# Optimization experiments

Measured on AMD Instinct MI355X. Metric: run time of the kernel, lower is better.

## Reference

```python
import jax, jax.numpy as jnp
import numpy as np

N_NODES = 20000
N_EDGES = 100000
IN = 512
HID = 512
OUT = 512
EF = 128
NH = 16
HEAD = OUT // NH


def _ln(x):
    mu = jnp.mean(x, axis=-1, keepdims=True)
    var = jnp.var(x, axis=-1, keepdims=True)
    return (x - mu) / jnp.sqrt(var + 1e-5)


def _mlp(x, W1, b1, g, be, W2, b2):
    hdn = x @ W1 + b1
    hdn = _ln(hdn) * g + be
    hdn = jax.nn.relu(hdn)
    return hdn @ W2 + b2


def setup_inputs() -> dict:
    key = jax.random.key(0)
    ks = jax.random.split(key, 16)

    def w(k, i, o):
        return jax.random.normal(k, (i, o), jnp.float32) / np.float32(np.sqrt(i))

    inp = {
        'h': jax.random.normal(ks[0], (N_NODES, IN), jnp.float32),
        'edge_feat': jax.random.normal(ks[1], (N_EDGES, EF), jnp.float32),
        'edge_index': jax.random.randint(ks[2], (2, N_EDGES), 0, N_NODES, jnp.int32),
    }
    # hk / hv MLPs: kv_input_dim = IN + EF
    inp['hk_W1'] = w(ks[3], IN + EF, HID); inp['hk_b1'] = jnp.zeros((HID,), jnp.float32)
    inp['hk_g'] = jnp.ones((HID,), jnp.float32); inp['hk_be'] = jnp.zeros((HID,), jnp.float32)
    inp['hk_W2'] = w(ks[4], HID, OUT); inp['hk_b2'] = jnp.zeros((OUT,), jnp.float32)
    inp['hv_W1'] = w(ks[5], IN + EF, HID); inp['hv_b1'] = jnp.zeros((HID,), jnp.float32)
    inp['hv_g'] = jnp.ones((HID,), jnp.float32); inp['hv_be'] = jnp.zeros((HID,), jnp.float32)
    inp['hv_W2'] = w(ks[6], HID, OUT); inp['hv_b2'] = jnp.zeros((OUT,), jnp.float32)
    # hq MLP: input_dim -> output_dim
    inp['hq_W1'] = w(ks[7], IN, HID); inp['hq_b1'] = jnp.zeros((HID,), jnp.float32)
    inp['hq_g'] = jnp.ones((HID,), jnp.float32); inp['hq_be'] = jnp.zeros((HID,), jnp.float32)
    inp['hq_W2'] = w(ks[8], HID, OUT); inp['hq_b2'] = jnp.zeros((OUT,), jnp.float32)
    # node_output MLP: 2*hidden -> hidden
    inp['no_W1'] = w(ks[9], 2 * HID, HID); inp['no_b1'] = jnp.zeros((HID,), jnp.float32)
    inp['no_g'] = jnp.ones((HID,), jnp.float32); inp['no_be'] = jnp.zeros((HID,), jnp.float32)
    inp['no_W2'] = w(ks[10], HID, HID); inp['no_b2'] = jnp.zeros((HID,), jnp.float32)
    return inp


def reference(h, edge_feat, edge_index,
              hk_W1, hk_b1, hk_g, hk_be, hk_W2, hk_b2,
              hv_W1, hv_b1, hv_g, hv_be, hv_W2, hv_b2,
              hq_W1, hq_b1, hq_g, hq_be, hq_W2, hq_b2,
              no_W1, no_b1, no_g, no_be, no_W2, no_b2):
    N = h.shape[0]
    src, dst = edge_index[0], edge_index[1]
    # edge gather + per-edge K/V MLPs
    kv_in = jnp.concatenate([h[src], edge_feat], axis=-1)          # [E, IN+EF]
    k = _mlp(kv_in, hk_W1, hk_b1, hk_g, hk_be, hk_W2, hk_b2).reshape(-1, NH, HEAD)
    v = _mlp(kv_in, hv_W1, hv_b1, hv_g, hv_be, hv_W2, hv_b2).reshape(-1, NH, HEAD)
    q = _mlp(h, hq_W1, hq_b1, hq_g, hq_be, hq_W2, hq_b2).reshape(-1, NH, HEAD)
    # scatter softmax over incoming edges of each dst node
    logits = jnp.sum(q[dst] * k, axis=-1) / np.float32(np.sqrt(HEAD))  # [E, NH]
    mx = jax.ops.segment_max(logits, dst, num_segments=N)              # [N, NH]
    ex = jnp.exp(logits - mx[dst])
    den = jax.ops.segment_sum(ex, dst, num_segments=N)                 # [N, NH]
    alpha = ex / den[dst]                                              # [E, NH]
    # scatter-sum aggregate
    m = alpha[..., None] * v                                           # [E, NH, HEAD]
    out = jax.ops.segment_sum(m, dst, num_segments=N).reshape(N, OUT)
    out = _mlp(jnp.concatenate([out, h], axis=-1), no_W1, no_b1, no_g, no_be, no_W2, no_b2)
    return out + h
```

## Files before the change

kernel.cpp:

```cpp
#include <hip/hip_runtime.h>

#define NN 20000
#define NE 100000

typedef unsigned short u16;
typedef __bf16 bf16x8 __attribute__((ext_vector_type(8)));
typedef float f32x4 __attribute__((ext_vector_type(4)));
typedef short short8 __attribute__((ext_vector_type(8)));
typedef u16 u16x4 __attribute__((ext_vector_type(4)));

__device__ __forceinline__ float bf2f(u16 u) {
    union { unsigned int i; float f; } x; x.i = ((unsigned int)u) << 16; return x.f;
}
__device__ __forceinline__ u16 f2bf(float f) {
    union { float f; unsigned int i; } x; x.f = f;
    unsigned int r = x.i + 0x7FFFu + ((x.i >> 16) & 1u);
    return (u16)(r >> 16);
}

__device__ __forceinline__ void gl_lds16(const void* g, void* l) {
    __builtin_amdgcn_global_load_lds(
        (__attribute__((address_space(1))) const void*)g,
        (__attribute__((address_space(3))) void*)l, 16, 0, 0);
}

__global__ void cvt_k(const float* __restrict__ in, u16* __restrict__ out, long n) {
    long i = ((long)blockIdx.x * 256 + threadIdx.x) * 4;
    if (i < n) {
        f32x4 v = *(const f32x4*)(in + i);
        u16x4 o;
        #pragma unroll
        for (int j = 0; j < 4; j++) o[j] = f2bf(v[j]);
        *(u16x4*)(out + i) = o;
    }
}

__global__ __launch_bounds__(256)
void ttr_k(const float* __restrict__ W, u16* __restrict__ WT, int Kr) {
    __shared__ float tile[32][33];
    int k0 = blockIdx.x * 32, n0 = blockIdx.y * 32;
    int tx = threadIdx.x & 31, ty = threadIdx.x >> 5;
    #pragma unroll
    for (int i = 0; i < 4; i++)
        tile[ty + 8 * i][tx] = W[(size_t)(k0 + ty + 8 * i) * 512 + n0 + tx];
    __syncthreads();
    #pragma unroll
    for (int i = 0; i < 4; i++)
        WT[(size_t)(n0 + ty + 8 * i) * Kr + k0 + tx] = f2bf(tile[tx][ty + 8 * i]);
}

template<int AK, bool BIAS, bool DEVM, bool OUTF, bool LOGIT>
__global__ __launch_bounds__(256, 2)
void gemm_k(const u16* __restrict__ A, const u16* __restrict__ A2,
            const int* __restrict__ eids, const int* __restrict__ Be, int ci, int cap,
            const u16* __restrict__ WT, const float* __restrict__ bias,
            void* __restrict__ Cv,
            const u16* __restrict__ qbv, const int* __restrict__ dstv, float* __restrict__ lgv,
            int Mh, int K, int Ast, int Cst)
{
    __shared__ u16 smem[128 * 128];
    u16* sA = smem;
    u16* sB = smem + 128 * 64;
    int M = Mh, b0 = 0;
    if constexpr (DEVM) {
        b0 = Be[ci];
        M = min(Be[ci + 1] - b0, cap);
    }
    const int m0 = blockIdx.y * 128;
    if (m0 >= M) return;
    const int t = threadIdx.x;
    const int n0 = blockIdx.x * 128;
    const int lane = t & 63;
    const int w = t >> 6;
    const int lrow = lane >> 3;
    const int swz = ((lane & 7) ^ lrow) * 8;
    const int ldst = w * 512 + lane * 8;

    size_t abase[4];
    #pragma unroll
    for (int p = 0; p < 4; p++) {
        int row = min(m0 + p * 32 + w * 8 + lrow, M - 1);
        if constexpr (AK == 2) abase[p] = (size_t)row * 512;
        else                   abase[p] = (size_t)row * Ast;
    }
    const int wm = w >> 1, wn = w & 1;
    const int lm = lane & 15, lk = lane >> 4;
    const int swzr = lm & 7;

    f32x4 acc[4][4] = {};

    for (int k0 = 0; k0 < K; k0 += 64) {
        #pragma unroll
        for (int p = 0; p < 4; p++) {
            const u16* g;
            if constexpr (AK == 2) {
                g = (k0 < 512) ? (A + abase[p] + k0 + swz) : (A2 + abase[p] + (k0 - 512) + swz);
            } else {
                g = A + abase[p] + k0 + swz;
            }
            gl_lds16(g, sA + p * 2048 + ldst);
        }
        #pragma unroll
        for (int p = 0; p < 4; p++)
            gl_lds16(WT + (size_t)(n0 + p * 32 + w * 8 + lrow) * K + k0 + swz, sB + p * 2048 + ldst);
        __syncthreads();

        bf16x8 av[2][4], bv[2][4];
        #pragma unroll
        for (int hf = 0; hf < 2; hf++) {
            #pragma unroll
            for (int mi = 0; mi < 4; mi++)
                av[hf][mi] = *(const bf16x8*)(sA + (wm * 64 + mi * 16 + lm) * 64 + (((hf * 4 + lk) ^ swzr) * 8));
            #pragma unroll
            for (int ni = 0; ni < 4; ni++)
                bv[hf][ni] = *(const bf16x8*)(sB + (wn * 64 + ni * 16 + lm) * 64 + (((hf * 4 + lk) ^ swzr) * 8));
        }
        #pragma unroll
        for (int hf = 0; hf < 2; hf++)
            #pragma unroll
            for (int mi = 0; mi < 4; mi++)
                #pragma unroll
                for (int ni = 0; ni < 4; ni++)
                    acc[mi][ni] = __builtin_amdgcn_mfma_f32_16x16x32_bf16(av[hf][mi], bv[hf][ni], acc[mi][ni], 0, 0, 0);
        __syncthreads();
    }

    float bvv[4];
    #pragma unroll
    for (int ni = 0; ni < 4; ni++) bvv[ni] = BIAS ? bias[n0 + wn * 64 + ni * 16 + lm] : 0.f;

    if constexpr (LOGIT) {
        const int qrow = t >> 4;
        const int qc = t & 15;
        #pragma unroll
        for (int p = 0; p < 8; p++) {
            int row = p * 16 + qrow;
            int grow = min(m0 + row, M - 1);
            int e = eids[b0 + grow];
            const u16* g = qbv + (size_t)dstv[e] * 512 + n0 + ((qc ^ (row & 7)) << 3);
            gl_lds16(g, smem + p * 2048 + t * 8);
        }
        __syncthreads();
        #pragma unroll
        for (int mi = 0; mi < 4; mi++) {
            #pragma unroll
            for (int r = 0; r < 4; r++) {
                int rloc = wm * 64 + mi * 16 + lk * 4 + r;
                float h0 = 0.f, h1 = 0.f;
                #pragma unroll
                for (int ni = 0; ni < 4; ni++) {
                    int cloc = wn * 64 + ni * 16 + lm;
                    int addr = rloc * 128 + ((((cloc >> 3) ^ (rloc & 7)) << 3) | (cloc & 7));
                    float qv = bf2f(smem[addr]);
                    float pr = (acc[mi][ni][r] + bvv[ni]) * qv;
                    if (ni < 2) h0 += pr; else h1 += pr;
                }
                #pragma unroll
                for (int o = 1; o < 16; o <<= 1) { h0 += __shfl_xor(h0, o); h1 += __shfl_xor(h1, o); }
                int grow = m0 + rloc;
                if (lm == 0 && grow < M) {
                    int hbase = (n0 >> 5) + wn * 2;
                    lgv[(size_t)(b0 + grow) * 16 + hbase]     = h0 * 0.17677669529663687f;
                    lgv[(size_t)(b0 + grow) * 16 + hbase + 1] = h1 * 0.17677669529663687f;
                }
            }
        }
        return;
    }

    #pragma unroll
    for (int mi = 0; mi < 4; mi++) {
        int rbase = m0 + wm * 64 + mi * 16 + lk * 4;
        #pragma unroll
        for (int ni = 0; ni < 4; ni++) {
            int n = n0 + wn * 64 + ni * 16 + lm;
            #pragma unroll
            for (int r = 0; r < 4; r++) {
                int row = rbase + r;
                if (row < M) {
                    float cv = acc[mi][ni][r] + bvv[ni];
                    if constexpr (OUTF) ((float*)Cv)[(size_t)row * Cst + n] = cv;
                    else                ((u16*)Cv)[(size_t)row * Cst + n] = f2bf(cv);
                }
            }
        }
    }
}

template<int AK, bool BIAS, bool RES, bool OUTF, bool RESB>
__global__ __launch_bounds__(256, 3)
void gemmS_k(const u16* __restrict__ A, const u16* __restrict__ A2,
             const u16* __restrict__ WT, const float* __restrict__ bias,
             const float* __restrict__ resid, void* __restrict__ Cv,
             int M, int K, int Ast, int Cst)
{
    __shared__ u16 sA[64 * 64];
    __shared__ u16 sB[128 * 64];
    const int m0 = blockIdx.y * 64;
    if (m0 >= M) return;
    const int t = threadIdx.x;
    const int n0 = blockIdx.x * 128;
    const int lane = t & 63;
    const int w = t >> 6;
    const int lrow = lane >> 3;
    const int swz = ((lane & 7) ^ lrow) * 8;
    const int ldst = w * 512 + lane * 8;

    size_t abase[2];
    #pragma unroll
    for (int p = 0; p < 2; p++) {
        int row = min(m0 + p * 32 + w * 8 + lrow, M - 1);
        if constexpr (AK == 2) abase[p] = (size_t)row * 512;
        else                   abase[p] = (size_t)row * Ast;
    }
    const int wm = w >> 1, wn = w & 1;
    const int lm = lane & 15, lk = lane >> 4;
    const int swzr = lm & 7;

    f32x4 acc[2][4] = {};

    for (int k0 = 0; k0 < K; k0 += 64) {
        #pragma unroll
        for (int p = 0; p < 2; p++) {
            const u16* g;
            if constexpr (AK == 2) {
                g = (k0 < 512) ? (A + abase[p] + k0 + swz) : (A2 + abase[p] + (k0 - 512) + swz);
            } else {
                g = A + abase[p] + k0 + swz;
            }
            gl_lds16(g, sA + p * 2048 + ldst);
        }
        #pragma unroll
        for (int p = 0; p < 4; p++)
            gl_lds16(WT + (size_t)(n0 + p * 32 + w * 8 + lrow) * K + k0 + swz, sB + p * 2048 + ldst);
        __syncthreads();

        bf16x8 av[2][2], bv[2][4];
        #pragma unroll
        for (int hf = 0; hf < 2; hf++) {
            #pragma unroll
            for (int mi = 0; mi < 2; mi++)
                av[hf][mi] = *(const bf16x8*)(sA + (wm * 32 + mi * 16 + lm) * 64 + (((hf * 4 + lk) ^ swzr) * 8));
            #pragma unroll
            for (int ni = 0; ni < 4; ni++)
                bv[hf][ni] = *(const bf16x8*)(sB + (wn * 64 + ni * 16 + lm) * 64 + (((hf * 4 + lk) ^ swzr) * 8));
        }
        #pragma unroll
        for (int hf = 0; hf < 2; hf++)
            #pragma unroll
            for (int mi = 0; mi < 2; mi++)
                #pragma unroll
                for (int ni = 0; ni < 4; ni++)
                    acc[mi][ni] = __builtin_amdgcn_mfma_f32_16x16x32_bf16(av[hf][mi], bv[hf][ni], acc[mi][ni], 0, 0, 0);
        __syncthreads();
    }

    float bvv[4];
    #pragma unroll
    for (int ni = 0; ni < 4; ni++) bvv[ni] = BIAS ? bias[n0 + wn * 64 + ni * 16 + lm] : 0.f;
    #pragma unroll
    for (int mi = 0; mi < 2; mi++) {
        int rbase = m0 + wm * 32 + mi * 16 + lk * 4;
        #pragma unroll
        for (int ni = 0; ni < 4; ni++) {
            int n = n0 + wn * 64 + ni * 16 + lm;
            #pragma unroll
            for (int r = 0; r < 4; r++) {
                int row = rbase + r;
                if (row < M) {
                    float cv = acc[mi][ni][r] + bvv[ni];
                    if constexpr (RES) {
                        if constexpr (RESB) cv += bf2f(((const u16*)resid)[(size_t)row * 512 + n]);
                        else                cv += resid[(size_t)row * 512 + n];
                    }
                    if constexpr (OUTF) ((float*)Cv)[(size_t)row * Cst + n] = cv;
                    else                ((u16*)Cv)[(size_t)row * Cst + n] = f2bf(cv);
                }
            }
        }
    }
}

__global__ __launch_bounds__(256, 2)
void g1ln_k(const u16* __restrict__ efb, const u16* __restrict__ WTe,
            const u16* __restrict__ NPp, const int* __restrict__ eids, const int* __restrict__ srcv,
            const int* __restrict__ Be, int ci, int cap,
            const float* __restrict__ b1, const float* __restrict__ g, const float* __restrict__ be,
            u16* __restrict__ outb)
{
    __shared__ u16 lds[4096 + 16384];
    u16* sA = lds;
    u16* sB = lds + 4096;
    float* sC = (float*)(lds + 4096);
    int b0 = Be[ci];
    int M = min(Be[ci + 1] - b0, cap);
    const int m0 = blockIdx.x * 32;
    if (m0 >= M) return;
    const int t = threadIdx.x;
    const int lane = t & 63;
    const int w = t >> 6;
    const int lm = lane & 15, lk = lane >> 4;

    #pragma unroll
    for (int p = 0; p < 2; p++) {
        int slot = p * 256 + t;
        int row = slot >> 4, gph = slot & 15;
        int gsrc = (gph & 8) | ((gph & 7) ^ (row & 7));
        int eid = eids[b0 + min(m0 + row, M - 1)];
        gl_lds16(efb + (size_t)eid * 128 + gsrc * 8, sA + slot * 8);
    }

    f32x4 acc[2][8] = {};
    for (int ks = 0; ks < 4; ks++) {
        #pragma unroll
        for (int p = 0; p < 8; p++) {
            int slot = p * 256 + t;
            int n = slot >> 2, cph = slot & 3;
            int csrc = cph ^ (n & 3);
            gl_lds16(WTe + (size_t)n * 128 + ks * 32 + csrc * 8, sB + slot * 8);
        }
        __syncthreads();
        bf16x8 av[2], bv[8];
        #pragma unroll
        for (int mi = 0; mi < 2; mi++) {
            int row = mi * 16 + lm;
            int gl = ks * 4 + lk;
            int gph = (gl & 8) | ((gl & 7) ^ (row & 7));
            av[mi] = *(const bf16x8*)(sA + row * 128 + gph * 8);
        }
        #pragma unroll
        for (int ni = 0; ni < 8; ni++) {
            int n = w * 128 + ni * 16 + lm;
            int cph = lk ^ (n & 3);
            bv[ni] = *(const bf16x8*)(sB + n * 32 + cph * 8);
        }
        #pragma unroll
        for (int mi = 0; mi < 2; mi++)
            #pragma unroll
            for (int ni = 0; ni < 8; ni++)
                acc[mi][ni] = __builtin_amdgcn_mfma_f32_16x16x32_bf16(av[mi], bv[ni], acc[mi][ni], 0, 0, 0);
        __syncthreads();
    }

    for (int half = 0; half < 2; half++) {
        #pragma unroll
        for (int ni = 0; ni < 8; ni++) {
            int col = w * 128 + ni * 16 + lm;
            int c4 = col >> 2;
            #pragma unroll
            for (int r = 0; r < 4; r++) {
                int row_l = lk * 4 + r;
                int ph4 = (c4 & ~7) | ((c4 & 7) ^ (row_l & 7));
                sC[row_l * 512 + ph4 * 4 + (col & 3)] = acc[half][ni][r];
            }
        }
        __syncthreads();
        #pragma unroll
        for (int i = 0; i < 4; i++) {
            int row_l = w * 4 + i;
            int row_g = m0 + half * 16 + row_l;
            if (row_g < M) {
                int g0 = lane * 2, g1 = g0 + 1;
                int p0 = (g0 & ~7) | ((g0 & 7) ^ (row_l & 7));
                int p1 = (g1 & ~7) | ((g1 & 7) ^ (row_l & 7));
                f32x4 ca = *(const f32x4*)(sC + row_l * 512 + p0 * 4);
                f32x4 cb = *(const f32x4*)(sC + row_l * 512 + p1 * 4);
                int eid = eids[b0 + row_g];
                const u16* gp = NPp + (size_t)srcv[eid] * 1536 + lane * 8;
                short8 gv = *(const short8*)gp;
                float x[8]; float s = 0.f, s2 = 0.f;
                #pragma unroll
                for (int j = 0; j < 4; j++) x[j] = ca[j] + bf2f((u16)gv[j]) + b1[lane * 8 + j];
                #pragma unroll
                for (int j = 4; j < 8; j++) x[j] = cb[j - 4] + bf2f((u16)gv[j]) + b1[lane * 8 + j];
                #pragma unroll
                for (int j = 0; j < 8; j++) { s += x[j]; s2 += x[j] * x[j]; }
                #pragma unroll
                for (int o = 32; o > 0; o >>= 1) { s += __shfl_xor(s, o); s2 += __shfl_xor(s2, o); }
                float mu = s * (1.f / 512.f);
                float inv = rsqrtf(s2 * (1.f / 512.f) - mu * mu + 1e-5f);
                short8 ov;
                #pragma unroll
                for (int j = 0; j < 8; j++) {
                    float y = (x[j] - mu) * inv * g[lane * 8 + j] + be[lane * 8 + j];
                    ov[j] = (short)f2bf(fmaxf(y, 0.f));
                }
                *(short8*)(outb + (size_t)row_g * 512 + lane * 8) = ov;
            }
        }
        __syncthreads();
    }
}

__global__ __launch_bounds__(256)
void ln_relu_k(u16* __restrict__ hid, int hst,
               const float* __restrict__ b1, const float* __restrict__ g, const float* __restrict__ be,
               int M) {
    int wid = threadIdx.x >> 6, lane = threadIdx.x & 63;
    long r = (long)blockIdx.x * 4 + wid;
    if (r >= M) return;
    u16* p = hid + r * hst + lane * 8;
    short8 v = *(const short8*)p;
    float x[8]; float s = 0.f, s2 = 0.f;
    #pragma unroll
    for (int j = 0; j < 8; j++) x[j] = bf2f((u16)v[j]) + b1[lane * 8 + j];
    #pragma unroll
    for (int j = 0; j < 8; j++) { s += x[j]; s2 += x[j] * x[j]; }
    #pragma unroll
    for (int o = 32; o > 0; o >>= 1) { s += __shfl_xor(s, o); s2 += __shfl_xor(s2, o); }
    float mu = s * (1.f / 512.f);
    float inv = rsqrtf(s2 * (1.f / 512.f) - mu * mu + 1e-5f);
    short8 ov;
    #pragma unroll
    for (int j = 0; j < 8; j++) {
        float y = (x[j] - mu) * inv * g[lane * 8 + j] + be[lane * 8 + j];
        ov[j] = (short)f2bf(fmaxf(y, 0.f));
    }
    *(short8*)p = ov;
}

__global__ void zero_k(int* a, int n) { int i = blockIdx.x * 256 + threadIdx.x; if (i < n) a[i] = 0; }
__global__ void count_k(const int* __restrict__ dst, int* __restrict__ counts) {
    int i = blockIdx.x * 256 + threadIdx.x;
    if (i < NE) atomicAdd(&counts[dst[i]], 1);
}
__global__ __launch_bounds__(1024)
void scan_k(const int* __restrict__ counts, int* __restrict__ offs) {
    __shared__ int part[1024];
    int t = threadIdx.x;
    const int chunk = (NN + 1023) / 1024;
    int lo = t * chunk; if (lo > NN) lo = NN;
    int hi = lo + chunk; if (hi > NN) hi = NN;
    int s = 0;
    for (int i = lo; i < hi; i++) s += counts[i];
    part[t] = s;
    __syncthreads();
    for (int o = 1; o < 1024; o <<= 1) {
        int v2 = 0;
        if (t >= o) v2 = part[t - o];
        __syncthreads();
        part[t] += v2;
        __syncthreads();
    }
    int base = (t > 0) ? part[t - 1] : 0;
    for (int i = lo; i < hi; i++) { offs[i] = base; base += counts[i]; }
    if (t == 1023) offs[NN] = part[1023];
}
__global__ void scatter_k(const int* __restrict__ dst, const int* __restrict__ offs,
                          int* __restrict__ cur, int* __restrict__ eids) {
    int i = blockIdx.x * 256 + threadIdx.x;
    if (i < NE) {
        int d = dst[i];
        int pos = atomicAdd(&cur[d], 1);
        eids[offs[d] + pos] = i;
    }
}
__global__ void bounds_k(const int* __restrict__ offs, int* __restrict__ Pn, int* __restrict__ Be,
                         int NC, int CEt) {
    int c = threadIdx.x;
    if (c > NC) return;
    int n;
    if (c == 0) n = 0;
    else if (c == NC) n = NN;
    else {
        int target = c * CEt;
        int lo = 0, hi = NN;
        while (lo < hi) { int mid = (lo + hi + 1) >> 1; if (offs[mid] <= target) lo = mid; else hi = mid - 1; }
        n = lo;
    }
    Pn[c] = n; Be[c] = offs[n];
}

__global__ __launch_bounds__(256)
void mxden_k(const float* __restrict__ lg, const int* __restrict__ offs,
             float* __restrict__ mx, float* __restrict__ den) {
    int wid = threadIdx.x >> 6, lane = threadIdx.x & 63;
    int n = blockIdx.x * 4 + wid;
    if (n >= NN) return;
    int lo = offs[n], hi = offs[n + 1];
    int head = lane & 15, j = lane >> 4;
    float m = -1e30f;
    for (int pe = lo + j; pe < hi; pe += 4)
        m = fmaxf(m, lg[(long)pe * 16 + head]);
    m = fmaxf(m, __shfl_xor(m, 16));
    m = fmaxf(m, __shfl_xor(m, 32));
    float d = 0.f;
    for (int pe = lo + j; pe < hi; pe += 4)
        d += __expf(lg[(long)pe * 16 + head] - m);
    d += __shfl_xor(d, 16);
    d += __shfl_xor(d, 32);
    if (j == 0) { mx[n * 16 + head] = m; den[n * 16 + head] = d; }
}

__global__ __launch_bounds__(256)
void aggc_k(const float* __restrict__ lg, const u16* __restrict__ v,
            const int* __restrict__ offs, const float* __restrict__ mx, const float* __restrict__ den,
            const int* __restrict__ Pn, const int* __restrict__ Be, int ci, int cap,
            u16* __restrict__ agg) {
    int wid = threadIdx.x >> 6, lane = threadIdx.x & 63;
    int n = blockIdx.x * 4 + wid;
    if (n >= NN) return;
    if (n < Pn[ci] || n >= Pn[ci + 1]) return;
    int lo = offs[n], hi = offs[n + 1], b0 = Be[ci];
    int head = lane >> 2;
    float m = mx[n * 16 + head];
    float dv = den[n * 16 + head];
    float rn = (hi > lo) ? (1.f / dv) : 0.f;
    float acc[8] = {0, 0, 0, 0, 0, 0, 0, 0};
    for (int pe = lo; pe < hi; pe++) {
        int r = pe - b0;
        if (r >= cap) break;
        float wgt = __expf(lg[(long)pe * 16 + head] - m);
        short8 vv = *(const short8*)(v + (long)r * 512 + lane * 8);
        #pragma unroll
        for (int j = 0; j < 8; j++) acc[j] += wgt * bf2f((u16)vv[j]);
    }
    short8 ov;
    #pragma unroll
    for (int j = 0; j < 8; j++) ov[j] = (short)f2bf(acc[j] * rn);
    *(short8*)(agg + (long)n * 512 + lane * 8) = ov;
}

extern "C" void kernel_launch(void* const* d_in, const int* in_sizes, int n_in,
                              void* d_out, int out_size, void* d_ws, size_t ws_size,
                              hipStream_t stream) {
    const float* h     = (const float*)d_in[0];
    const float* efeat = (const float*)d_in[1];
    const int*   eidx  = (const int*)d_in[2];
    const int* src = eidx;
    const int* dst = eidx + NE;
    const float* hkW1 = (const float*)d_in[3];  const float* hkb1 = (const float*)d_in[4];
    const float* hkg  = (const float*)d_in[5];  const float* hkbe = (const float*)d_in[6];
    const float* hkW2 = (const float*)d_in[7];  const float* hkb2 = (const float*)d_in[8];
    const float* hvW1 = (const float*)d_in[9];  const float* hvb1 = (const float*)d_in[10];
    const float* hvg  = (const float*)d_in[11]; const float* hvbe = (const float*)d_in[12];
    const float* hvW2 = (const float*)d_in[13]; const float* hvb2 = (const float*)d_in[14];
    const float* hqW1 = (const float*)d_in[15]; const float* hqb1 = (const float*)d_in[16];
    const float* hqg  = (const float*)d_in[17]; const float* hqbe = (const float*)d_in[18];
    const float* hqW2 = (const float*)d_in[19]; const float* hqb2 = (const float*)d_in[20];
    const float* noW1 = (const float*)d_in[21]; const float* nob1 = (const float*)d_in[22];
    const float* nog  = (const float*)d_in[23]; const float* nobe = (const float*)d_in[24];
    const float* noW2 = (const float*)d_in[25]; const float* nob2 = (const float*)d_in[26];
    (void)in_sizes; (void)n_in; (void)out_size;

    char* wsp = (char*)d_ws;
    auto take = [&](size_t b) -> char* {
        char* r = wsp; wsp += (b + 255) & ~(size_t)255; return r;
    };
    u16* hb    = (u16*)take((size_t)NN * 512 * 2);
    u16* efb   = (u16*)take((size_t)NE * 128 * 2);
    u16* qb    = (u16*)take((size_t)NN * 512 * 2);
    u16* aggb  = (u16*)take((size_t)NN * 512 * 2);
    u16* NP    = (u16*)take((size_t)NN * 1536 * 2);
    float* lgb = (float*)take((size_t)NE * 16 * 4);
    float* mxb = (float*)take((size_t)NN * 16 * 4);
    float* denb= (float*)take((size_t)NN * 16 * 4);
    u16* WTn    = (u16*)take((size_t)1536 * 512 * 2);
    u16* noW1T  = (u16*)take(512 * 1024 * 2);
    u16* hkW1Te = (u16*)take(512 * 128 * 2);
    u16* hvW1Te = (u16*)take(512 * 128 * 2);
    u16* hkW2T  = (u16*)take(512 * 512 * 2);
    u16* hvW2T  = (u16*)take(512 * 512 * 2);
    u16* hqW2T  = (u16*)take(512 * 512 * 2);
    u16* noW2T  = (u16*)take(512 * 512 * 2);
    int* counts = (int*)take(NN * 4);
    int* offs   = (int*)take((NN + 1) * 4);
    int* cur    = (int*)take(NN * 4);
    int* eids   = (int*)take(NE * 4);
    int* Pn     = (int*)take(64 * 4);
    int* Bed    = (int*)take(64 * 4);

    size_t base = (size_t)(wsp - (char*)d_ws);
    const int ncs[15] = {1, 2, 3, 4, 5, 6, 8, 10, 13, 16, 20, 25, 32, 40, 50};
    int NC = 50;
    size_t cap = (size_t)((NE + 49) / 50) + 2048;
    for (int i = 0; i < 15; i++) {
        int nc = ncs[i];
        int cet = (NE + nc - 1) / nc;
        size_t c2 = (nc == 1) ? (size_t)NE : (size_t)cet + 2048;
        size_t buf = (c2 * 1024 + 255) & ~(size_t)255;
        if (base + 2 * buf <= ws_size) { NC = nc; cap = c2; break; }
    }
    size_t chunkbuf = (cap * 1024 + 255) & ~(size_t)255;
    u16* hidC = (u16*)take(chunkbuf);
    u16* kvC  = (u16*)take(chunkbuf);
    const int icap = (int)cap;
    const int CEt = (NE + NC - 1) / NC;

    cvt_k<<<((NN * 512 / 4) + 255) / 256, 256, 0, stream>>>(h, hb, (long)NN * 512);
    cvt_k<<<((NE * 128 / 4) + 255) / 256, 256, 0, stream>>>(efeat, efb, (long)NE * 128);

    dim3 tb(256);
    ttr_k<<<dim3(16, 16), tb, 0, stream>>>(hqW1, WTn, 512);
    ttr_k<<<dim3(16, 16), tb, 0, stream>>>(hkW1, WTn + 512 * 512, 512);
    ttr_k<<<dim3(16, 16), tb, 0, stream>>>(hvW1, WTn + 2 * 512 * 512, 512);
    ttr_k<<<dim3(4, 16),  tb, 0, stream>>>(hkW1 + 512 * 512, hkW1Te, 128);
    ttr_k<<<dim3(4, 16),  tb, 0, stream>>>(hvW1 + 512 * 512, hvW1Te, 128);
    ttr_k<<<dim3(32, 16), tb, 0, stream>>>(noW1, noW1T, 1024);
    ttr_k<<<dim3(16, 16), tb, 0, stream>>>(hkW2, hkW2T, 512);
    ttr_k<<<dim3(16, 16), tb, 0, stream>>>(hvW2, hvW2T, 512);
    ttr_k<<<dim3(16, 16), tb, 0, stream>>>(hqW2, hqW2T, 512);
    ttr_k<<<dim3(16, 16), tb, 0, stream>>>(noW2, noW2T, 512);

    zero_k<<<(NN + 255) / 256, 256, 0, stream>>>(counts, NN);
    zero_k<<<(NN + 255) / 256, 256, 0, stream>>>(cur, NN);
    count_k<<<(NE + 255) / 256, 256, 0, stream>>>(dst, counts);
    scan_k<<<1, 1024, 0, stream>>>(counts, offs);
    scatter_k<<<(NE + 255) / 256, 256, 0, stream>>>(dst, offs, cur, eids);
    bounds_k<<<1, 64, 0, stream>>>(offs, Pn, Bed, NC, CEt);

    dim3 gNP(12, (NN + 127) / 128);
    dim3 gNS(4, (NN + 63) / 64);
    dim3 gC(4, ((int)cap + 127) / 128);
    int lnN = (NN + 3) / 4;
    int g1b = ((int)cap + 31) / 32;

    gemm_k<0, false, false, false, false><<<gNP, 256, 0, stream>>>(
        hb, nullptr, nullptr, nullptr, 0, 0, WTn, nullptr, NP,
        nullptr, nullptr, nullptr, NN, 512, 512, 1536);

    ln_relu_k<<<lnN, 256, 0, stream>>>(NP, 1536, hqb1, hqg, hqbe, NN);
    gemmS_k<0, true, false, false, false><<<gNS, 256, 0, stream>>>(NP, nullptr, hqW2T, hqb2, nullptr, qb,
                                                                   NN, 512, 1536, 512);

    for (int c = 0; c < NC; c++) {
        g1ln_k<<<g1b, 256, 0, stream>>>(efb, hkW1Te, NP + 512, eids, src, Bed, c, icap,
                                        hkb1, hkg, hkbe, hidC);
        gemm_k<0, true, true, false, true><<<gC, 256, 0, stream>>>(
            hidC, nullptr, eids, Bed, c, icap, hkW2T, hkb2, nullptr,
            qb, dst, lgb, 0, 512, 512, 512);
    }

    mxden_k<<<lnN, 256, 0, stream>>>(lgb, offs, mxb, denb);

    for (int c = 0; c < NC; c++) {
        g1ln_k<<<g1b, 256, 0, stream>>>(efb, hvW1Te, NP + 1024, eids, src, Bed, c, icap,
                                        hvb1, hvg, hvbe, hidC);
        gemm_k<0, true, true, false, false><<<gC, 256, 0, stream>>>(
            hidC, nullptr, nullptr, Bed, c, icap, hvW2T, hvb2, kvC,
            nullptr, nullptr, nullptr, 0, 512, 512, 512);
        aggc_k<<<lnN, 256, 0, stream>>>(lgb, kvC, offs, mxb, denb, Pn, Bed, c, icap, aggb);
    }

    gemmS_k<2, false, false, false, false><<<gNS, 256, 0, stream>>>(aggb, hb, noW1T, nullptr, nullptr, qb,
                                                                    NN, 1024, 512, 512);
    ln_relu_k<<<lnN, 256, 0, stream>>>(qb, 512, nob1, nog, nobe, NN);
    gemmS_k<0, true, true, true, true><<<gNS, 256, 0, stream>>>(qb, nullptr, noW2T, nob2, (const float*)hb, d_out,
                                                                NN, 512, 512, 512);
}
```

Before: 749.8 us.

## Add XCD-aware block swizzle to GEMMs and enlarge g1ln tile to 64 rows

Remaps workgroup IDs in both GEMM kernels so that consecutive tiles land on the same XCD, aiming to improve L2 reuse of shared A and B panels. The edge-feature GEMM+LayerNorm kernel now uses 512 threads and 64-row tiles with a 4x4 MFMA layout per wave instead of 32 rows and 256 threads. This halves the number of blocks and reuses each loaded W tile across twice as many rows. The larger LDS footprint (64KB) and block size may reduce occupancy, and sC now aliases sA.

```diff
diff --git a/kernel.cpp b/kernel.cpp
--- a/kernel.cpp
+++ b/kernel.cpp
@@ -22,6 +22,16 @@
     __builtin_amdgcn_global_load_lds(
         (__attribute__((address_space(1))) const void*)g,
         (__attribute__((address_space(3))) void*)l, 16, 0, 0);
+}
+
+__device__ __forceinline__ void xcd_swz(int& x, int& y) {
+    int gx = gridDim.x;
+    int nwg = gx * gridDim.y;
+    int bid = blockIdx.y * gx + blockIdx.x;
+    int q = nwg >> 3, r = nwg & 7;
+    int xcd = bid & 7, idx = bid >> 3;
+    int wg = (xcd < r ? xcd * (q + 1) : r * (q + 1) + (xcd - r) * q) + idx;
+    x = wg % gx; y = wg / gx;
 }
 
 __global__ void cvt_k(const float* __restrict__ in, u16* __restrict__ out, long n) {
@@ -66,10 +76,12 @@
         b0 = Be[ci];
         M = min(Be[ci + 1] - b0, cap);
     }
-    const int m0 = blockIdx.y * 128;
+    int bx, by;
+    xcd_swz(bx, by);
+    const int m0 = by * 128;
     if (m0 >= M) return;
     const int t = threadIdx.x;
-    const int n0 = blockIdx.x * 128;
+    const int n0 = bx * 128;
     const int lane = t & 63;
     const int w = t >> 6;
     const int lrow = lane >> 3;
@@ -196,10 +208,12 @@
 {
     __shared__ u16 sA[64 * 64];
     __shared__ u16 sB[128 * 64];
-    const int m0 = blockIdx.y * 64;
+    int bx, by;
+    xcd_swz(bx, by);
+    const int m0 = by * 64;
     if (m0 >= M) return;
     const int t = threadIdx.x;
-    const int n0 = blockIdx.x * 128;
+    const int n0 = bx * 128;
     const int lane = t & 63;
     const int w = t >> 6;
     const int lrow = lane >> 3;
@@ -281,20 +295,20 @@
     }
 }
 
-__global__ __launch_bounds__(256, 2)
+__global__ __launch_bounds__(512, 4)
 void g1ln_k(const u16* __restrict__ efb, const u16* __restrict__ WTe,
             const u16* __restrict__ NPp, const int* __restrict__ eids, const int* __restrict__ srcv,
             const int* __restrict__ Be, int ci, int cap,
             const float* __restrict__ b1, const float* __restrict__ g, const float* __restrict__ be,
             u16* __restrict__ outb)
 {
-    __shared__ u16 lds[4096 + 16384];
+    __shared__ u16 lds[32768];
     u16* sA = lds;
-    u16* sB = lds + 4096;
-    float* sC = (float*)(lds + 4096);
+    u16* sB = lds + 8192;
+    float* sC = (float*)lds;
     int b0 = Be[ci];
     int M = min(Be[ci + 1] - b0, cap);
-    const int m0 = blockIdx.x * 32;
+    const int m0 = blockIdx.x * 64;
     if (m0 >= M) return;
     const int t = threadIdx.x;
     const int lane = t & 63;
@@ -303,62 +317,65 @@
 
     #pragma unroll
     for (int p = 0; p < 2; p++) {
-        int slot = p * 256 + t;
+        int slot = p * 512 + t;
         int row = slot >> 4, gph = slot & 15;
         int gsrc = (gph & 8) | ((gph & 7) ^ (row & 7));
         int eid = eids[b0 + min(m0 + row, M - 1)];
         gl_lds16(efb + (size_t)eid * 128 + gsrc * 8, sA + slot * 8);
     }
 
-    f32x4 acc[2][8] = {};
+    f32x4 acc[4][4] = {};
     for (int ks = 0; ks < 4; ks++) {
         #pragma unroll
-        for (int p = 0; p < 8; p++) {
-            int slot = p * 256 + t;
+        for (int p = 0; p < 4; p++) {
+            int slot = p * 512 + t;
             int n = slot >> 2, cph = slot & 3;
             int csrc = cph ^ (n & 3);
             gl_lds16(WTe + (size_t)n * 128 + ks * 32 + csrc * 8, sB + slot * 8);
         }
         __syncthreads();
-        bf16x8 av[2], bv[8];
-        #pragma unroll
-        for (int mi = 0; mi < 2; mi++) {
+        bf16x8 av[4], bv[4];
+        #pragma unroll
+        for (int mi = 0; mi < 4; mi++) {
             int row = mi * 16 + lm;
             int gl = ks * 4 + lk;
             int gph = (gl & 8) | ((gl & 7) ^ (row & 7));
             av[mi] = *(const bf16x8*)(sA + row * 128 + gph * 8);
         }
         #pragma unroll
-        for (int ni = 0; ni < 8; ni++) {
-            int n = w * 128 + ni * 16 + lm;
-            int cph = lk ^ (n & 3);
-            bv[ni] = *(const bf16x8*)(sB + n * 32 + cph * 8);
-        }
-        #pragma unroll
-        for (int mi = 0; mi < 2; mi++)
-            #pragma unroll
-            for (int ni = 0; ni < 8; ni++)
+        for (int ni = 0; ni < 4; ni++) {
+            int n = w * 64 + ni * 16 + lm;
+            bv[ni] = *(const bf16x8*)(sB + n * 32 + (lk ^ (n & 3)) * 8);
+        }
+        #pragma unroll
+        for (int mi = 0; mi < 4; mi++)
+            #pragma unroll
+            for (int ni = 0; ni < 4; ni++)
                 acc[mi][ni] = __builtin_amdgcn_mfma_f32_16x16x32_bf16(av[mi], bv[ni], acc[mi][ni], 0, 0, 0);
         __syncthreads();
     }
 
     for (int half = 0; half < 2; half++) {
         #pragma unroll
-        for (int ni = 0; ni < 8; ni++) {
-            int col = w * 128 + ni * 16 + lm;
-            int c4 = col >> 2;
-            #pragma unroll
-            for (int r = 0; r < 4; r++) {
-                int row_l = lk * 4 + r;
-                int ph4 = (c4 & ~7) | ((c4 & 7) ^ (row_l & 7));
-                sC[row_l * 512 + ph4 * 4 + (col & 3)] = acc[half][ni][r];
+        for (int mi2 = 0; mi2 < 2; mi2++) {
+            int mi = half * 2 + mi2;
+            #pragma unroll
+            for (int ni = 0; ni < 4; ni++) {
+                int col = w * 64 + ni * 16 + lm;
+                int c4 = col >> 2;
+                #pragma unroll
+                for (int r = 0; r < 4; r++) {
+                    int row_l = mi2 * 16 + lk * 4 + r;
+                    int ph4 = (c4 & ~7) | ((c4 & 7) ^ (row_l & 7));
+                    sC[row_l * 512 + ph4 * 4 + (col & 3)] = acc[mi][ni][r];
+                }
             }
         }
         __syncthreads();
         #pragma unroll
         for (int i = 0; i < 4; i++) {
             int row_l = w * 4 + i;
-            int row_g = m0 + half * 16 + row_l;
+            int row_g = m0 + half * 32 + row_l;
             if (row_g < M) {
                 int g0 = lane * 2, g1 = g0 + 1;
                 int p0 = (g0 & ~7) | ((g0 & 7) ^ (row_l & 7));
@@ -613,7 +630,7 @@
     dim3 gNS(4, (NN + 63) / 64);
     dim3 gC(4, ((int)cap + 127) / 128);
     int lnN = (NN + 3) / 4;
-    int g1b = ((int)cap + 31) / 32;
+    int g1b = ((int)cap + 63) / 64;
 
     gemm_k<0, false, false, false, false><<<gNP, 256, 0, stream>>>(
         hb, nullptr, nullptr, nullptr, 0, 0, WTn, nullptr, NP,
@@ -624,7 +641,7 @@
                                                                    NN, 512, 1536, 512);
 
     for (int c = 0; c < NC; c++) {
-        g1ln_k<<<g1b, 256, 0, stream>>>(efb, hkW1Te, NP + 512, eids, src, Bed, c, icap,
+        g1ln_k<<<g1b, 512, 0, stream>>>(efb, hkW1Te, NP + 512, eids, src, Bed, c, icap,
                                         hkb1, hkg, hkbe, hidC);
         gemm_k<0, true, true, false, true><<<gC, 256, 0, stream>>>(
             hidC, nullptr, eids, Bed, c, icap, hkW2T, hkb2, nullptr,
@@ -634,7 +651,7 @@
     mxden_k<<<lnN, 256, 0, stream>>>(lgb, offs, mxb, denb);
 
     for (int c = 0; c < NC; c++) {
-        g1ln_k<<<g1b, 256, 0, stream>>>(efb, hvW1Te, NP + 1024, eids, src, Bed, c, icap,
+        g1ln_k<<<g1b, 512, 0, stream>>>(efb, hvW1Te, NP + 1024, eids, src, Bed, c, icap,
                                         hvb1, hvg, hvbe, hidC);
         gemm_k<0, true, true, false, false><<<gC, 256, 0, stream>>>(
             hidC, nullptr, nullptr, Bed, c, icap, hvW2T, hvb2, kvC,
```

Result: faster. 708.5 us (-5.5%).
